# Optimization experiments

Measured on AMD Instinct MI355X. Metric: run time of the kernel, lower is better.

## Reference

```python
import jax, jax.numpy as jnp
import numpy as np

HEADS = 8
DIM_HEAD = 64
DIM_INNER = HEADS * DIM_HEAD  # 512
SCALE = DIM_HEAD ** -0.5
B, N, D = 8, 512, 512
NEG = -1e9


def setup_inputs() -> dict:
    key = jax.random.key(0)
    ks = jax.random.split(key, 12)
    inp = {}
    for i in range(3):
        inp[f"x{i}"] = jax.random.normal(ks[i], (B, N, D), dtype=jnp.float32)
        inp[f"m{i}"] = jax.random.randint(ks[3 + i], (B, N), 0, 2).astype(bool)
        inp[f"Wqkv{i}"] = jax.random.normal(ks[6 + i], (D, 3 * DIM_INNER), dtype=jnp.float32) * 0.02
        inp[f"Wout{i}"] = jax.random.normal(ks[9 + i], (DIM_INNER, D), dtype=jnp.float32) * 0.02
    return inp


def _split_heads(t):
    # [b, n, h*d] -> [b, h, n, d]
    b, n, _ = t.shape
    return t.reshape(b, n, HEADS, DIM_HEAD).transpose(0, 2, 1, 3)


def _forward(xs, masks, Wqkvs, Wouts):
    qs, ks, vs = [], [], []
    for x, W in zip(xs, Wqkvs):
        q, k, v = jnp.split(x @ W, 3, axis=-1)
        qs.append(_split_heads(q))
        ks.append(_split_heads(k))
        vs.append(_split_heads(v))
    K = jnp.concatenate(ks, axis=2)  # [b, h, 3n, d]
    V = jnp.concatenate(vs, axis=2)
    outs = []
    for q, m, Wo in zip(qs, masks, Wouts):
        dots = jnp.einsum('bhnd,bhmd->bhnm', q, K) * SCALE
        # original masks whole query rows: masked_fill(~mask[:, None, :, None], -1e9)
        dots = jnp.where(m[:, None, :, None], dots, NEG)
        attn = jax.nn.softmax(dots, axis=-1)  # dropout is identity at eval
        o = jnp.einsum('bhnm,bhmd->bhnd', attn, V)
        o = o.transpose(0, 2, 1, 3).reshape(q.shape[0], q.shape[2], DIM_INNER)
        outs.append(o @ Wo)
    return tuple(outs)


def reference(x0, x1, x2, m0, m1, m2, Wqkv0, Wqkv1, Wqkv2, Wout0, Wout1, Wout2):
    return _forward((x0, x1, x2), (m0, m1, m2), (Wqkv0, Wqkv1, Wqkv2), (Wout0, Wout1, Wout2))
```

## Files before the change

kernel.cpp:

```cpp
#include <hip/hip_runtime.h>
#include <cstdint>
#include <cstddef>

#define NEGV  -1.0e9f
#define QSCALE 0.18033688011112042f

typedef _Float16 h8 __attribute__((ext_vector_type(8)));
typedef _Float16 h4 __attribute__((ext_vector_type(4)));
typedef float    f4 __attribute__((ext_vector_type(4)));


static __device__ inline h8 cvt8(float4 a, float4 b) {
    h8 r = { (_Float16)a.x, (_Float16)a.y, (_Float16)a.z, (_Float16)a.w,
             (_Float16)b.x, (_Float16)b.y, (_Float16)b.z, (_Float16)b.w };
    return r;
}

__global__ __launch_bounds__(256) void tr_cvt(
    const float* __restrict__ s0, const float* __restrict__ s1, const float* __restrict__ s2,
    _Float16* __restrict__ dst, int R, int C)
{
    const int mod = blockIdx.z;
    const float* __restrict__ s = (mod == 0) ? s0 : ((mod == 1) ? s1 : s2);
    _Float16* __restrict__ d = dst + (size_t)mod * R * C;
    const int c0 = blockIdx.x * 32, r0 = blockIdx.y * 32;
    __shared__ float tile[32][33];
    const int tr = threadIdx.x >> 3;
    const int tc = (threadIdx.x & 7) * 4;
    float4 v = *reinterpret_cast<const float4*>(&s[(size_t)(r0 + tr) * C + c0 + tc]);
    tile[tr][tc + 0] = v.x; tile[tr][tc + 1] = v.y; tile[tr][tc + 2] = v.z; tile[tr][tc + 3] = v.w;
    __syncthreads();
    h4 o = { (_Float16)tile[tc + 0][tr], (_Float16)tile[tc + 1][tr],
             (_Float16)tile[tc + 2][tr], (_Float16)tile[tc + 3][tr] };
    *reinterpret_cast<h4*>(&d[(size_t)(c0 + tr) * R + r0 + tc]) = o;
}

__global__ __launch_bounds__(256) void qkv_gemm_f16(
    const float* __restrict__ x0, const float* __restrict__ x1, const float* __restrict__ x2,
    const _Float16* __restrict__ Wqt,
    _Float16* __restrict__ Qh, _Float16* __restrict__ Kh, _Float16* __restrict__ Vt)
{
    const int mod = blockIdx.z;
    const float* __restrict__ A = (mod == 0) ? x0 : ((mod == 1) ? x1 : x2);
    const _Float16* __restrict__ Bw = Wqt + (size_t)mod * 1536 * 512;

    __shared__ _Float16 smem[2 * 128 * 40];
    _Float16* As = smem;
    _Float16* Bs = smem + 128 * 40;

    const int t = threadIdx.x;
    const int brow = blockIdx.x * 128, bcol = blockIdx.y * 128;
    const int w = t >> 6, l = t & 63;
    const int wr = (w >> 1) * 64, wc = (w & 1) * 64;
    const int lr = l & 15, lk = (l >> 4) * 8, lg = l >> 4;

    const int sm0 = t >> 2, skk = (t & 3) * 8, sm1 = sm0 + 64;

    f4 acc[4][4] = {};
    float4 axr[2][2];
    h8 brg[2];

    axr[0][0] = *reinterpret_cast<const float4*>(&A[(size_t)(brow + sm0) * 512 + skk]);
    axr[0][1] = *reinterpret_cast<const float4*>(&A[(size_t)(brow + sm0) * 512 + skk + 4]);
    axr[1][0] = *reinterpret_cast<const float4*>(&A[(size_t)(brow + sm1) * 512 + skk]);
    axr[1][1] = *reinterpret_cast<const float4*>(&A[(size_t)(brow + sm1) * 512 + skk + 4]);
    brg[0] = *reinterpret_cast<const h8*>(&Bw[(size_t)(bcol + sm0) * 512 + skk]);
    brg[1] = *reinterpret_cast<const h8*>(&Bw[(size_t)(bcol + sm1) * 512 + skk]);
    *reinterpret_cast<h8*>(&As[sm0 * 40 + skk]) = cvt8(axr[0][0], axr[0][1]);
    *reinterpret_cast<h8*>(&As[sm1 * 40 + skk]) = cvt8(axr[1][0], axr[1][1]);
    *reinterpret_cast<h8*>(&Bs[sm0 * 40 + skk]) = brg[0];
    *reinterpret_cast<h8*>(&Bs[sm1 * 40 + skk]) = brg[1];

    for (int k0 = 0; k0 < 512; k0 += 32) {
        __syncthreads();
        const bool more = (k0 + 32) < 512;
        if (more) {
            const int kn = k0 + 32 + skk;
            axr[0][0] = *reinterpret_cast<const float4*>(&A[(size_t)(brow + sm0) * 512 + kn]);
            axr[0][1] = *reinterpret_cast<const float4*>(&A[(size_t)(brow + sm0) * 512 + kn + 4]);
            axr[1][0] = *reinterpret_cast<const float4*>(&A[(size_t)(brow + sm1) * 512 + kn]);
            axr[1][1] = *reinterpret_cast<const float4*>(&A[(size_t)(brow + sm1) * 512 + kn + 4]);
            brg[0] = *reinterpret_cast<const h8*>(&Bw[(size_t)(bcol + sm0) * 512 + k0 + 32 + skk]);
            brg[1] = *reinterpret_cast<const h8*>(&Bw[(size_t)(bcol + sm1) * 512 + k0 + 32 + skk]);
        }
        h8 af[4], bf[4];
#pragma unroll
        for (int m = 0; m < 4; m++)
            af[m] = *reinterpret_cast<h8*>(&As[(wr + m * 16 + lr) * 40 + lk]);
#pragma unroll
        for (int n = 0; n < 4; n++)
            bf[n] = *reinterpret_cast<h8*>(&Bs[(wc + n * 16 + lr) * 40 + lk]);
        __builtin_amdgcn_s_setprio(1);
#pragma unroll
        for (int m = 0; m < 4; m++)
#pragma unroll
            for (int n = 0; n < 4; n++)
                acc[m][n] = __builtin_amdgcn_mfma_f32_16x16x32_f16(af[m], bf[n], acc[m][n], 0, 0, 0);
        __builtin_amdgcn_s_setprio(0);
        __syncthreads();
        if (more) {
            *reinterpret_cast<h8*>(&As[sm0 * 40 + skk]) = cvt8(axr[0][0], axr[0][1]);
            *reinterpret_cast<h8*>(&As[sm1 * 40 + skk]) = cvt8(axr[1][0], axr[1][1]);
            *reinterpret_cast<h8*>(&Bs[sm0 * 40 + skk]) = brg[0];
            *reinterpret_cast<h8*>(&Bs[sm1 * 40 + skk]) = brg[1];
        }
    }

    const int sec = bcol >> 9;
    const int b = brow >> 9;
    const int nbase = brow & 511;
    const int cbase = bcol - (sec << 9);

    if (sec == 2) {
#pragma unroll
        for (int m = 0; m < 4; m++) {
            const int n = nbase + wr + m * 16 + lg * 4;
#pragma unroll
            for (int nn = 0; nn < 4; nn++) {
                const int cis = cbase + wc + nn * 16 + lr;
                const int hh = cis >> 6, d = cis & 63;
                h4 pv = { (_Float16)acc[m][nn][0], (_Float16)acc[m][nn][1],
                          (_Float16)acc[m][nn][2], (_Float16)acc[m][nn][3] };
                *reinterpret_cast<h4*>(&Vt[(((size_t)b * 8 + hh) * 64 + d) * 1536 + mod * 512 + n]) = pv;
            }
        }
    } else {
        const float scl = (sec == 0) ? QSCALE : 1.0f;
        _Float16 (*Ts)[136] = reinterpret_cast<_Float16(*)[136]>(smem);
#pragma unroll
        for (int pass = 0; pass < 2; pass++) {
            __syncthreads();
            if ((w >> 1) == pass) {
#pragma unroll
                for (int m = 0; m < 4; m++)
#pragma unroll
                    for (int nn = 0; nn < 4; nn++)
#pragma unroll
                        for (int reg = 0; reg < 4; reg++)
                            Ts[m * 16 + lg * 4 + reg][wc + nn * 16 + lr] =
                                (_Float16)(acc[m][nn][reg] * scl);
            }
            __syncthreads();
#pragma unroll
            for (int it = 0; it < 4; it++) {
                const int idx = t + it * 256;
                const int r = idx >> 4, c = (idx & 15) * 8;
                h8 v = *reinterpret_cast<h8*>(&Ts[r][c]);
                const int n = nbase + pass * 64 + r;
                const int cis = cbase + c;
                const int hh = cis >> 6, d = cis & 63;
                if (sec == 0)
                    *reinterpret_cast<h8*>(&Qh[((((size_t)mod * 8 + b) * 8 + hh) * 512 + n) * 64 + d]) = v;
                else
                    *reinterpret_cast<h8*>(&Kh[(((size_t)b * 8 + hh) * 1536 + mod * 512 + n) * 64 + d]) = v;
            }
        }
    }
}

__global__ __launch_bounds__(512) void attn_f16(
    const _Float16* __restrict__ Qh, const _Float16* __restrict__ Kh, const _Float16* __restrict__ Vt,
    const int* __restrict__ m0, const int* __restrict__ m1, const int* __restrict__ m2,
    _Float16* __restrict__ Oh)
{
    const int mod = blockIdx.z;
    const int bh = blockIdx.x, b = bh >> 3, h = bh & 7;
    const int q0 = blockIdx.y * 128;

    __shared__ _Float16 Ks[64 * 72];
    __shared__ _Float16 Vs[64 * 72];
    __shared__ _Float16 Ps[128 * 72];

    const int t = threadIdx.x, w = t >> 6, l = t & 63;
    const int lr = l & 15, lg = l >> 4, lk = lg * 8;

    const _Float16* __restrict__ Qp = Qh + ((((size_t)mod * 8 + b) * 8 + h) * 512 + q0 + w * 16) * 64;
    h8 qf0 = *reinterpret_cast<const h8*>(&Qp[(size_t)lr * 64 + lk]);
    h8 qf1 = *reinterpret_cast<const h8*>(&Qp[(size_t)lr * 64 + 32 + lk]);

    const int* __restrict__ mk = (mod == 0) ? m0 : ((mod == 1) ? m1 : m2);
    const bool msk = mk[b * 512 + q0 + w * 16 + lr] != 0;

    float mrow = -3.0e38f, lsum = 0.f;
    f4 o[4] = {};

    const int sr = t >> 3, skk = (t & 7) * 8;
    const _Float16* __restrict__ kSrc = Kh + (size_t)bh * 1536 * 64 + (size_t)sr * 64 + skk;
    const _Float16* __restrict__ vSrc = Vt + (size_t)bh * 64 * 1536 + (size_t)sr * 1536 + skk;
    _Float16* kDst = &Ks[sr * 72 + skk];
    _Float16* vDst = &Vs[sr * 72 + skk];

    h8 krg = *reinterpret_cast<const h8*>(kSrc);
    h8 vrg = *reinterpret_cast<const h8*>(vSrc);
    *reinterpret_cast<h8*>(kDst) = krg;
    *reinterpret_cast<h8*>(vDst) = vrg;

    for (int c0 = 0; c0 < 1536; c0 += 64) {
        __syncthreads();
        const bool more = (c0 + 64) < 1536;
        if (more) {
            krg = *reinterpret_cast<const h8*>(kSrc + (size_t)(c0 + 64) * 64);
            vrg = *reinterpret_cast<const h8*>(vSrc + (c0 + 64));
        }

        f4 st[4] = {};
        __builtin_amdgcn_s_setprio(1);
#pragma unroll
        for (int kb = 0; kb < 4; kb++) {
            h8 ka0 = *reinterpret_cast<h8*>(&Ks[(kb * 16 + lr) * 72 + lk]);
            h8 ka1 = *reinterpret_cast<h8*>(&Ks[(kb * 16 + lr) * 72 + 32 + lk]);
            st[kb] = __builtin_amdgcn_mfma_f32_16x16x32_f16(ka0, qf0, st[kb], 0, 0, 0);
            st[kb] = __builtin_amdgcn_mfma_f32_16x16x32_f16(ka1, qf1, st[kb], 0, 0, 0);
        }
        __builtin_amdgcn_s_setprio(0);

        if (!msk) {
#pragma unroll
            for (int kb = 0; kb < 4; kb++) { st[kb][0] = NEGV; st[kb][1] = NEGV; st[kb][2] = NEGV; st[kb][3] = NEGV; }
        }
        float cm = fmaxf(fmaxf(fmaxf(st[0][0], st[0][1]), fmaxf(st[0][2], st[0][3])),
                         fmaxf(fmaxf(st[1][0], st[1][1]), fmaxf(st[1][2], st[1][3])));
        cm = fmaxf(cm, fmaxf(fmaxf(fmaxf(st[2][0], st[2][1]), fmaxf(st[2][2], st[2][3])),
                             fmaxf(fmaxf(st[3][0], st[3][1]), fmaxf(st[3][2], st[3][3]))));
        cm = fmaxf(cm, __shfl_xor(cm, 16));
        cm = fmaxf(cm, __shfl_xor(cm, 32));

        if (!__all(cm <= mrow + 8.0f)) {
            const float mn = fmaxf(mrow, cm);
            const float sc = __builtin_amdgcn_exp2f(mrow - mn);
            mrow = mn;
            lsum *= sc;
#pragma unroll
            for (int dg = 0; dg < 4; dg++) o[dg] *= sc;
        }

        float rs = 0.f;
#pragma unroll
        for (int kb = 0; kb < 4; kb++) {
            const float p0 = __builtin_amdgcn_exp2f(st[kb][0] - mrow);
            const float p1 = __builtin_amdgcn_exp2f(st[kb][1] - mrow);
            const float p2 = __builtin_amdgcn_exp2f(st[kb][2] - mrow);
            const float p3 = __builtin_amdgcn_exp2f(st[kb][3] - mrow);
            rs += (p0 + p1) + (p2 + p3);
            h4 ph = { (_Float16)p0, (_Float16)p1, (_Float16)p2, (_Float16)p3 };
            *reinterpret_cast<h4*>(&Ps[(w * 16 + lr) * 72 + kb * 16 + lg * 4]) = ph;
        }
        rs += __shfl_xor(rs, 16);
        rs += __shfl_xor(rs, 32);
        lsum += rs;

        __builtin_amdgcn_s_setprio(1);
#pragma unroll
        for (int kb2 = 0; kb2 < 2; kb2++) {
            h8 pa = *reinterpret_cast<h8*>(&Ps[(w * 16 + lr) * 72 + kb2 * 32 + lk]);
#pragma unroll
            for (int dg = 0; dg < 4; dg++) {
                h8 va = *reinterpret_cast<h8*>(&Vs[(dg * 16 + lr) * 72 + kb2 * 32 + lk]);
                o[dg] = __builtin_amdgcn_mfma_f32_16x16x32_f16(va, pa, o[dg], 0, 0, 0);
            }
        }
        __builtin_amdgcn_s_setprio(0);

        __syncthreads();
        if (more) {
            *reinterpret_cast<h8*>(kDst) = krg;
            *reinterpret_cast<h8*>(vDst) = vrg;
        }
    }

    const float inv = 1.f / lsum;
    const size_t row = (size_t)mod * 4096 + b * 512 + q0 + w * 16 + lr;
#pragma unroll
    for (int dg = 0; dg < 4; dg++) {
        h4 ov = { (_Float16)(o[dg][0] * inv), (_Float16)(o[dg][1] * inv),
                  (_Float16)(o[dg][2] * inv), (_Float16)(o[dg][3] * inv) };
        *reinterpret_cast<h4*>(&Oh[row * 512 + h * 64 + dg * 16 + lg * 4]) = ov;
    }
}

__global__ __launch_bounds__(256) void out_gemm_f16(
    const _Float16* __restrict__ Oh, const _Float16* __restrict__ Wot,
    float* __restrict__ out)
{
    const int mod = blockIdx.z;
    const _Float16* __restrict__ A  = Oh  + (size_t)mod * 4096 * 512;
    const _Float16* __restrict__ Bw = Wot + (size_t)mod * 512 * 512;
    float* __restrict__ C = out + (size_t)mod * 4096 * 512;

    __shared__ _Float16 As[128 * 40];
    __shared__ _Float16 Bs[128 * 40];

    const int t = threadIdx.x;
    const int brow = blockIdx.x * 128, bcol = blockIdx.y * 128;
    const int w = t >> 6, l = t & 63;
    const int wr = (w >> 1) * 64, wc = (w & 1) * 64;
    const int lr = l & 15, lk = (l >> 4) * 8, lg = l >> 4;

    const int sm0 = t >> 2, skk = (t & 3) * 8, sm1 = sm0 + 64;

    f4 acc[4][4] = {};
    h8 arg[2], brg[2];

    arg[0] = *reinterpret_cast<const h8*>(&A [(size_t)(brow + sm0) * 512 + skk]);
    arg[1] = *reinterpret_cast<const h8*>(&A [(size_t)(brow + sm1) * 512 + skk]);
    brg[0] = *reinterpret_cast<const h8*>(&Bw[(size_t)(bcol + sm0) * 512 + skk]);
    brg[1] = *reinterpret_cast<const h8*>(&Bw[(size_t)(bcol + sm1) * 512 + skk]);
    *reinterpret_cast<h8*>(&As[sm0 * 40 + skk]) = arg[0];
    *reinterpret_cast<h8*>(&As[sm1 * 40 + skk]) = arg[1];
    *reinterpret_cast<h8*>(&Bs[sm0 * 40 + skk]) = brg[0];
    *reinterpret_cast<h8*>(&Bs[sm1 * 40 + skk]) = brg[1];

    for (int k0 = 0; k0 < 512; k0 += 32) {
        __syncthreads();
        const bool more = (k0 + 32) < 512;
        if (more) {
            const int kn = k0 + 32 + skk;
            arg[0] = *reinterpret_cast<const h8*>(&A [(size_t)(brow + sm0) * 512 + kn]);
            arg[1] = *reinterpret_cast<const h8*>(&A [(size_t)(brow + sm1) * 512 + kn]);
            brg[0] = *reinterpret_cast<const h8*>(&Bw[(size_t)(bcol + sm0) * 512 + kn]);
            brg[1] = *reinterpret_cast<const h8*>(&Bw[(size_t)(bcol + sm1) * 512 + kn]);
        }
        h8 af[4], bf[4];
#pragma unroll
        for (int m = 0; m < 4; m++)
            af[m] = *reinterpret_cast<h8*>(&As[(wr + m * 16 + lr) * 40 + lk]);
#pragma unroll
        for (int n = 0; n < 4; n++)
            bf[n] = *reinterpret_cast<h8*>(&Bs[(wc + n * 16 + lr) * 40 + lk]);
        __builtin_amdgcn_s_setprio(1);
#pragma unroll
        for (int m = 0; m < 4; m++)
#pragma unroll
            for (int n = 0; n < 4; n++)
                acc[m][n] = __builtin_amdgcn_mfma_f32_16x16x32_f16(af[m], bf[n], acc[m][n], 0, 0, 0);
        __builtin_amdgcn_s_setprio(0);
        __syncthreads();
        if (more) {
            *reinterpret_cast<h8*>(&As[sm0 * 40 + skk]) = arg[0];
            *reinterpret_cast<h8*>(&As[sm1 * 40 + skk]) = arg[1];
            *reinterpret_cast<h8*>(&Bs[sm0 * 40 + skk]) = brg[0];
            *reinterpret_cast<h8*>(&Bs[sm1 * 40 + skk]) = brg[1];
        }
    }

#pragma unroll
    for (int m = 0; m < 4; m++) {
        const int rloc = wr + m * 16 + lg * 4;
#pragma unroll
        for (int reg = 0; reg < 4; reg++) {
            const size_t base = (size_t)(brow + rloc + reg) * 512 + bcol;
#pragma unroll
            for (int nn = 0; nn < 4; nn++)
                C[base + wc + nn * 16 + lr] = acc[m][nn][reg];
        }
    }
}

extern "C" void kernel_launch(void* const* d_in, const int* in_sizes, int n_in,
                              void* d_out, int out_size, void* d_ws, size_t ws_size,
                              hipStream_t stream)
{
    const float* x0  = (const float*)d_in[0];
    const int*   m0  = (const int*)  d_in[1];
    const float* Wq0 = (const float*)d_in[2];
    const float* Wo0 = (const float*)d_in[3];
    const float* x1  = (const float*)d_in[4];
    const int*   m1  = (const int*)  d_in[5];
    const float* Wq1 = (const float*)d_in[6];
    const float* Wo1 = (const float*)d_in[7];
    const float* x2  = (const float*)d_in[8];
    const int*   m2  = (const int*)  d_in[9];
    const float* Wq2 = (const float*)d_in[10];
    const float* Wo2 = (const float*)d_in[11];

    _Float16* Wqt = (_Float16*)d_ws;
    _Float16* Wot = Wqt + 2359296;
    _Float16* Qh  = Wot + 786432;
    _Float16* Kh  = Qh  + 6291456;
    _Float16* Vt  = Kh  + 6291456;
    _Float16* Oh  = Vt  + 6291456;

    tr_cvt<<<dim3(48, 16, 3), 256, 0, stream>>>(Wq0, Wq1, Wq2, Wqt, 512, 1536);
    tr_cvt<<<dim3(16, 16, 3), 256, 0, stream>>>(Wo0, Wo1, Wo2, Wot, 512, 512);

    qkv_gemm_f16<<<dim3(32, 12, 3), 256, 0, stream>>>(x0, x1, x2, Wqt, Qh, Kh, Vt);
    attn_f16    <<<dim3(64, 4, 3), 512, 0, stream>>>(Qh, Kh, Vt, m0, m1, m2, Oh);
    out_gemm_f16<<<dim3(32, 4, 3), 256, 0, stream>>>(Oh, Wot, (float*)d_out);
}
```

Before: 230.7 us.

## Merge weight conversion launches, deepen GEMM K-tiles, shrink out-GEMM row tile

Combines the two weight transpose/convert kernels into a single launch. Both GEMMs now stage a K-step of 64 instead of 32, which halves the number of barrier pairs per tile and issues wider global loads per thread. The output GEMM uses 64-row tiles so it launches twice as many blocks for better occupancy on the CU count. In exchange the kernels use more shared memory and registers, and the smaller output tile gives less reuse of the weight tile.

```diff
diff --git a/kernel.cpp b/kernel.cpp
--- a/kernel.cpp
+++ b/kernel.cpp
@@ -16,14 +16,26 @@
     return r;
 }
 
-__global__ __launch_bounds__(256) void tr_cvt(
-    const float* __restrict__ s0, const float* __restrict__ s1, const float* __restrict__ s2,
-    _Float16* __restrict__ dst, int R, int C)
+__global__ __launch_bounds__(256) void wt_cvt(
+    const float* __restrict__ q0, const float* __restrict__ q1, const float* __restrict__ q2,
+    const float* __restrict__ o0, const float* __restrict__ o1, const float* __restrict__ o2,
+    _Float16* __restrict__ Wqt, _Float16* __restrict__ Wot)
 {
     const int mod = blockIdx.z;
-    const float* __restrict__ s = (mod == 0) ? s0 : ((mod == 1) ? s1 : s2);
-    _Float16* __restrict__ d = dst + (size_t)mod * R * C;
-    const int c0 = blockIdx.x * 32, r0 = blockIdx.y * 32;
+    const int flat = blockIdx.x;
+    const float* s;
+    _Float16* d;
+    int C, bx, by;
+    if (flat < 768) {
+        C = 1536; bx = flat % 48; by = flat / 48;
+        s = (mod == 0) ? q0 : ((mod == 1) ? q1 : q2);
+        d = Wqt + (size_t)mod * 1536 * 512;
+    } else {
+        C = 512; bx = (flat - 768) % 16; by = (flat - 768) / 16;
+        s = (mod == 0) ? o0 : ((mod == 1) ? o1 : o2);
+        d = Wot + (size_t)mod * 512 * 512;
+    }
+    const int c0 = bx * 32, r0 = by * 32;
     __shared__ float tile[32][33];
     const int tr = threadIdx.x >> 3;
     const int tc = (threadIdx.x & 7) * 4;
@@ -32,7 +44,7 @@
     __syncthreads();
     h4 o = { (_Float16)tile[tc + 0][tr], (_Float16)tile[tc + 1][tr],
              (_Float16)tile[tc + 2][tr], (_Float16)tile[tc + 3][tr] };
-    *reinterpret_cast<h4*>(&d[(size_t)(c0 + tr) * R + r0 + tc]) = o;
+    *reinterpret_cast<h4*>(&d[(size_t)(c0 + tr) * 512 + r0 + tc]) = o;
 }
 
 __global__ __launch_bounds__(256) void qkv_gemm_f16(
@@ -44,65 +56,70 @@
     const float* __restrict__ A = (mod == 0) ? x0 : ((mod == 1) ? x1 : x2);
     const _Float16* __restrict__ Bw = Wqt + (size_t)mod * 1536 * 512;
 
-    __shared__ _Float16 smem[2 * 128 * 40];
+    __shared__ _Float16 smem[2 * 128 * 72];
     _Float16* As = smem;
-    _Float16* Bs = smem + 128 * 40;
+    _Float16* Bs = smem + 128 * 72;
 
     const int t = threadIdx.x;
     const int brow = blockIdx.x * 128, bcol = blockIdx.y * 128;
     const int w = t >> 6, l = t & 63;
     const int wr = (w >> 1) * 64, wc = (w & 1) * 64;
-    const int lr = l & 15, lk = (l >> 4) * 8, lg = l >> 4;
-
-    const int sm0 = t >> 2, skk = (t & 3) * 8, sm1 = sm0 + 64;
+    const int lr = l & 15, lg = l >> 4, lk = lg * 8;
+
+    const int sm = t >> 1, sk = (t & 1) * 32;
+    const float*    __restrict__ aRow = &A [(size_t)(brow + sm) * 512 + sk];
+    const _Float16* __restrict__ bRow = &Bw[(size_t)(bcol + sm) * 512 + sk];
+    _Float16* aDst = &As[sm * 72 + sk];
+    _Float16* bDst = &Bs[sm * 72 + sk];
 
     f4 acc[4][4] = {};
-    float4 axr[2][2];
-    h8 brg[2];
-
-    axr[0][0] = *reinterpret_cast<const float4*>(&A[(size_t)(brow + sm0) * 512 + skk]);
-    axr[0][1] = *reinterpret_cast<const float4*>(&A[(size_t)(brow + sm0) * 512 + skk + 4]);
-    axr[1][0] = *reinterpret_cast<const float4*>(&A[(size_t)(brow + sm1) * 512 + skk]);
-    axr[1][1] = *reinterpret_cast<const float4*>(&A[(size_t)(brow + sm1) * 512 + skk + 4]);
-    brg[0] = *reinterpret_cast<const h8*>(&Bw[(size_t)(bcol + sm0) * 512 + skk]);
-    brg[1] = *reinterpret_cast<const h8*>(&Bw[(size_t)(bcol + sm1) * 512 + skk]);
-    *reinterpret_cast<h8*>(&As[sm0 * 40 + skk]) = cvt8(axr[0][0], axr[0][1]);
-    *reinterpret_cast<h8*>(&As[sm1 * 40 + skk]) = cvt8(axr[1][0], axr[1][1]);
-    *reinterpret_cast<h8*>(&Bs[sm0 * 40 + skk]) = brg[0];
-    *reinterpret_cast<h8*>(&Bs[sm1 * 40 + skk]) = brg[1];
-
-    for (int k0 = 0; k0 < 512; k0 += 32) {
-        __syncthreads();
-        const bool more = (k0 + 32) < 512;
-        if (more) {
-            const int kn = k0 + 32 + skk;
-            axr[0][0] = *reinterpret_cast<const float4*>(&A[(size_t)(brow + sm0) * 512 + kn]);
-            axr[0][1] = *reinterpret_cast<const float4*>(&A[(size_t)(brow + sm0) * 512 + kn + 4]);
-            axr[1][0] = *reinterpret_cast<const float4*>(&A[(size_t)(brow + sm1) * 512 + kn]);
-            axr[1][1] = *reinterpret_cast<const float4*>(&A[(size_t)(brow + sm1) * 512 + kn + 4]);
-            brg[0] = *reinterpret_cast<const h8*>(&Bw[(size_t)(bcol + sm0) * 512 + k0 + 32 + skk]);
-            brg[1] = *reinterpret_cast<const h8*>(&Bw[(size_t)(bcol + sm1) * 512 + k0 + 32 + skk]);
-        }
-        h8 af[4], bf[4];
-#pragma unroll
-        for (int m = 0; m < 4; m++)
-            af[m] = *reinterpret_cast<h8*>(&As[(wr + m * 16 + lr) * 40 + lk]);
-#pragma unroll
-        for (int n = 0; n < 4; n++)
-            bf[n] = *reinterpret_cast<h8*>(&Bs[(wc + n * 16 + lr) * 40 + lk]);
-        __builtin_amdgcn_s_setprio(1);
-#pragma unroll
-        for (int m = 0; m < 4; m++)
+    float4 ax[8];
+    h8 bx[4];
+
+#pragma unroll
+    for (int j = 0; j < 8; j++) ax[j] = *reinterpret_cast<const float4*>(&aRow[j * 4]);
+#pragma unroll
+    for (int j = 0; j < 4; j++) bx[j] = *reinterpret_cast<const h8*>(&bRow[j * 8]);
+#pragma unroll
+    for (int j = 0; j < 4; j++) {
+        *reinterpret_cast<h8*>(&aDst[j * 8]) = cvt8(ax[2 * j], ax[2 * j + 1]);
+        *reinterpret_cast<h8*>(&bDst[j * 8]) = bx[j];
+    }
+
+    for (int k0 = 0; k0 < 512; k0 += 64) {
+        __syncthreads();
+        const bool more = (k0 + 64) < 512;
+        if (more) {
+            const int kn = k0 + 64;
+#pragma unroll
+            for (int j = 0; j < 8; j++) ax[j] = *reinterpret_cast<const float4*>(&aRow[kn + j * 4]);
+#pragma unroll
+            for (int j = 0; j < 4; j++) bx[j] = *reinterpret_cast<const h8*>(&bRow[kn + j * 8]);
+        }
+#pragma unroll
+        for (int ks = 0; ks < 64; ks += 32) {
+            h8 af[4], bf[4];
+#pragma unroll
+            for (int m = 0; m < 4; m++)
+                af[m] = *reinterpret_cast<h8*>(&As[(wr + m * 16 + lr) * 72 + ks + lk]);
 #pragma unroll
             for (int n = 0; n < 4; n++)
-                acc[m][n] = __builtin_amdgcn_mfma_f32_16x16x32_f16(af[m], bf[n], acc[m][n], 0, 0, 0);
-        __builtin_amdgcn_s_setprio(0);
-        __syncthreads();
-        if (more) {
-            *reinterpret_cast<h8*>(&As[sm0 * 40 + skk]) = cvt8(axr[0][0], axr[0][1]);
-            *reinterpret_cast<h8*>(&As[sm1 * 40 + skk]) = cvt8(axr[1][0], axr[1][1]);
-            *reinterpret_cast<h8*>(&Bs[sm0 * 40 + skk]) = brg[0];
-            *reinterpret_cast<h8*>(&Bs[sm1 * 40 + skk]) = brg[1];
+                bf[n] = *reinterpret_cast<h8*>(&Bs[(wc + n * 16 + lr) * 72 + ks + lk]);
+            __builtin_amdgcn_s_setprio(1);
+#pragma unroll
+            for (int m = 0; m < 4; m++)
+#pragma unroll
+                for (int n = 0; n < 4; n++)
+                    acc[m][n] = __builtin_amdgcn_mfma_f32_16x16x32_f16(af[m], bf[n], acc[m][n], 0, 0, 0);
+            __builtin_amdgcn_s_setprio(0);
+        }
+        __syncthreads();
+        if (more) {
+#pragma unroll
+            for (int j = 0; j < 4; j++) {
+                *reinterpret_cast<h8*>(&aDst[j * 8]) = cvt8(ax[2 * j], ax[2 * j + 1]);
+                *reinterpret_cast<h8*>(&bDst[j * 8]) = bx[j];
+            }
         }
     }
 
@@ -287,64 +304,73 @@
     const _Float16* __restrict__ Bw = Wot + (size_t)mod * 512 * 512;
     float* __restrict__ C = out + (size_t)mod * 4096 * 512;
 
-    __shared__ _Float16 As[128 * 40];
-    __shared__ _Float16 Bs[128 * 40];
+    __shared__ _Float16 smem[(64 + 128) * 72];
+    _Float16* As = smem;
+    _Float16* Bs = smem + 64 * 72;
 
     const int t = threadIdx.x;
-    const int brow = blockIdx.x * 128, bcol = blockIdx.y * 128;
+    const int brow = blockIdx.x * 64, bcol = blockIdx.y * 128;
     const int w = t >> 6, l = t & 63;
-    const int wr = (w >> 1) * 64, wc = (w & 1) * 64;
-    const int lr = l & 15, lk = (l >> 4) * 8, lg = l >> 4;
-
-    const int sm0 = t >> 2, skk = (t & 3) * 8, sm1 = sm0 + 64;
-
-    f4 acc[4][4] = {};
-    h8 arg[2], brg[2];
-
-    arg[0] = *reinterpret_cast<const h8*>(&A [(size_t)(brow + sm0) * 512 + skk]);
-    arg[1] = *reinterpret_cast<const h8*>(&A [(size_t)(brow + sm1) * 512 + skk]);
-    brg[0] = *reinterpret_cast<const h8*>(&Bw[(size_t)(bcol + sm0) * 512 + skk]);
-    brg[1] = *reinterpret_cast<const h8*>(&Bw[(size_t)(bcol + sm1) * 512 + skk]);
-    *reinterpret_cast<h8*>(&As[sm0 * 40 + skk]) = arg[0];
-    *reinterpret_cast<h8*>(&As[sm1 * 40 + skk]) = arg[1];
-    *reinterpret_cast<h8*>(&Bs[sm0 * 40 + skk]) = brg[0];
-    *reinterpret_cast<h8*>(&Bs[sm1 * 40 + skk]) = brg[1];
-
-    for (int k0 = 0; k0 < 512; k0 += 32) {
-        __syncthreads();
-        const bool more = (k0 + 32) < 512;
-        if (more) {
-            const int kn = k0 + 32 + skk;
-            arg[0] = *reinterpret_cast<const h8*>(&A [(size_t)(brow + sm0) * 512 + kn]);
-            arg[1] = *reinterpret_cast<const h8*>(&A [(size_t)(brow + sm1) * 512 + kn]);
-            brg[0] = *reinterpret_cast<const h8*>(&Bw[(size_t)(bcol + sm0) * 512 + kn]);
-            brg[1] = *reinterpret_cast<const h8*>(&Bw[(size_t)(bcol + sm1) * 512 + kn]);
-        }
-        h8 af[4], bf[4];
-#pragma unroll
-        for (int m = 0; m < 4; m++)
-            af[m] = *reinterpret_cast<h8*>(&As[(wr + m * 16 + lr) * 40 + lk]);
-#pragma unroll
-        for (int n = 0; n < 4; n++)
-            bf[n] = *reinterpret_cast<h8*>(&Bs[(wc + n * 16 + lr) * 40 + lk]);
-        __builtin_amdgcn_s_setprio(1);
-#pragma unroll
-        for (int m = 0; m < 4; m++)
+    const int wr = (w >> 1) * 32, wc = (w & 1) * 64;
+    const int lr = l & 15, lg = l >> 4, lk = lg * 8;
+
+    const int sa = t >> 2, ska = (t & 3) * 16;
+    const int sb = t >> 1, skb = (t & 1) * 32;
+    const _Float16* __restrict__ aRow = &A [(size_t)(brow + sa) * 512 + ska];
+    const _Float16* __restrict__ bRow = &Bw[(size_t)(bcol + sb) * 512 + skb];
+    _Float16* aDst = &As[sa * 72 + ska];
+    _Float16* bDst = &Bs[sb * 72 + skb];
+
+    f4 acc[2][4] = {};
+    h8 axr[2], bxr[4];
+
+#pragma unroll
+    for (int j = 0; j < 2; j++) axr[j] = *reinterpret_cast<const h8*>(&aRow[j * 8]);
+#pragma unroll
+    for (int j = 0; j < 4; j++) bxr[j] = *reinterpret_cast<const h8*>(&bRow[j * 8]);
+#pragma unroll
+    for (int j = 0; j < 2; j++) *reinterpret_cast<h8*>(&aDst[j * 8]) = axr[j];
+#pragma unroll
+    for (int j = 0; j < 4; j++) *reinterpret_cast<h8*>(&bDst[j * 8]) = bxr[j];
+
+    for (int k0 = 0; k0 < 512; k0 += 64) {
+        __syncthreads();
+        const bool more = (k0 + 64) < 512;
+        if (more) {
+            const int kn = k0 + 64;
+#pragma unroll
+            for (int j = 0; j < 2; j++) axr[j] = *reinterpret_cast<const h8*>(&aRow[kn + j * 8]);
+#pragma unroll
+            for (int j = 0; j < 4; j++) bxr[j] = *reinterpret_cast<const h8*>(&bRow[kn + j * 8]);
+        }
+#pragma unroll
+        for (int ks = 0; ks < 64; ks += 32) {
+            h8 af[2], bf[4];
+#pragma unroll
+            for (int m = 0; m < 2; m++)
+                af[m] = *reinterpret_cast<h8*>(&As[(wr + m * 16 + lr) * 72 + ks + lk]);
 #pragma unroll
             for (int n = 0; n < 4; n++)
-                acc[m][n] = __builtin_amdgcn_mfma_f32_16x16x32_f16(af[m], bf[n], acc[m][n], 0, 0, 0);
-        __builtin_amdgcn_s_setprio(0);
-        __syncthreads();
-        if (more) {
-            *reinterpret_cast<h8*>(&As[sm0 * 40 + skk]) = arg[0];
-            *reinterpret_cast<h8*>(&As[sm1 * 40 + skk]) = arg[1];
-            *reinterpret_cast<h8*>(&Bs[sm0 * 40 + skk]) = brg[0];
-            *reinterpret_cast<h8*>(&Bs[sm1 * 40 + skk]) = brg[1];
-        }
-    }
-
-#pragma unroll
-    for (int m = 0; m < 4; m++) {
+                bf[n] = *reinterpret_cast<h8*>(&Bs[(wc + n * 16 + lr) * 72 + ks + lk]);
+            __builtin_amdgcn_s_setprio(1);
+#pragma unroll
+            for (int m = 0; m < 2; m++)
+#pragma unroll
+                for (int n = 0; n < 4; n++)
+                    acc[m][n] = __builtin_amdgcn_mfma_f32_16x16x32_f16(af[m], bf[n], acc[m][n], 0, 0, 0);
+            __builtin_amdgcn_s_setprio(0);
+        }
+        __syncthreads();
+        if (more) {
+#pragma unroll
+            for (int j = 0; j < 2; j++) *reinterpret_cast<h8*>(&aDst[j * 8]) = axr[j];
+#pragma unroll
+            for (int j = 0; j < 4; j++) *reinterpret_cast<h8*>(&bDst[j * 8]) = bxr[j];
+        }
+    }
+
+#pragma unroll
+    for (int m = 0; m < 2; m++) {
         const int rloc = wr + m * 16 + lg * 4;
 #pragma unroll
         for (int reg = 0; reg < 4; reg++) {
@@ -380,10 +406,8 @@
     _Float16* Vt  = Kh  + 6291456;
     _Float16* Oh  = Vt  + 6291456;
 
-    tr_cvt<<<dim3(48, 16, 3), 256, 0, stream>>>(Wq0, Wq1, Wq2, Wqt, 512, 1536);
-    tr_cvt<<<dim3(16, 16, 3), 256, 0, stream>>>(Wo0, Wo1, Wo2, Wot, 512, 512);
-
+    wt_cvt<<<dim3(1024, 1, 3), 256, 0, stream>>>(Wq0, Wq1, Wq2, Wo0, Wo1, Wo2, Wqt, Wot);
     qkv_gemm_f16<<<dim3(32, 12, 3), 256, 0, stream>>>(x0, x1, x2, Wqt, Qh, Kh, Vt);
     attn_f16    <<<dim3(64, 4, 3), 512, 0, stream>>>(Qh, Kh, Vt, m0, m1, m2, Oh);
-    out_gemm_f16<<<dim3(32, 4, 3), 256, 0, stream>>>(Oh, Wot, (float*)d_out);
-}
+    out_gemm_f16<<<dim3(64, 4, 3), 256, 0, stream>>>(Oh, Wot, (float*)d_out);
+}
```

Measured after the change: 236.3 us. 1.02x slower.
